# Optimization experiments

Measured on AMD Instinct MI355X. Metric: run time of the kernel, lower is better.

The kernel has to match this reference:

```python
import jax, jax.numpy as jnp
import numpy as np

EPS = 1e-5
NUM_HEADS = 8
KEY_DIM = 32
V_DIM = 128  # att_ratio * key_dim

def bn2d(x, g, b, m, v):
    # inference BatchNorm2d on NCHW
    s = g * jax.lax.rsqrt(v + EPS)
    return x * s[None, :, None, None] + (b - m * s)[None, :, None, None]

def conv1x1(x, w):
    # w: [out_c, in_c], x: [B,C,H,W]
    return jnp.einsum('oc,bchw->bohw', w, x)

def _bn_params(key, c):
    k1, k2, k3, k4 = jax.random.split(key, 4)
    g = jax.random.uniform(k1, (c,), jnp.float32, 0.5, 1.5)
    b = jax.random.normal(k2, (c,), jnp.float32) * 0.1
    m = jax.random.normal(k3, (c,), jnp.float32) * 0.1
    v = jax.random.uniform(k4, (c,), jnp.float32, 0.5, 1.5)
    return g, b, m, v

def setup_inputs() -> dict:
    key = jax.random.key(0)
    ks = jax.random.split(key, 12)
    inp_dim, out_dim = 256, 512
    kv_out = (KEY_DIM + V_DIM) * NUM_HEADS      # 1280
    q_out = KEY_DIM * NUM_HEADS                 # 256
    merge_dim = V_DIM * NUM_HEADS               # 1024
    hid = out_dim * 2                            # mlp_ratio=2 -> 1024
    d = {}
    d['x'] = jax.random.normal(ks[0], (32, inp_dim, 32, 32), jnp.float32)
    d['kv_w'] = jax.random.normal(ks[1], (kv_out, inp_dim), jnp.float32) * 0.02
    d['kv_g'], d['kv_b'], d['kv_m'], d['kv_v'] = _bn_params(ks[2], kv_out)
    d['q_w'] = jax.random.normal(ks[3], (q_out, inp_dim), jnp.float32) * 0.02
    d['q_g'], d['q_b'], d['q_m'], d['q_v'] = _bn_params(ks[4], q_out)
    d['mg_w'] = jax.random.normal(ks[5], (out_dim, merge_dim), jnp.float32) * 0.02
    d['mg_g'], d['mg_b'], d['mg_m'], d['mg_v'] = _bn_params(ks[6], out_dim)
    d['fc1_w'] = jax.random.normal(ks[7], (hid, out_dim), jnp.float32) * 0.02
    d['bn1_g'], d['bn1_b'], d['bn1_m'], d['bn1_v'] = _bn_params(ks[8], hid)
    d['fc2_w'] = jax.random.normal(ks[9], (out_dim, hid), jnp.float32) * 0.02
    d['bn2_g'], d['bn2_b'], d['bn2_m'], d['bn2_v'] = _bn_params(ks[10], out_dim)
    return d

def reference(x, kv_w, kv_g, kv_b, kv_m, kv_v, q_w, q_g, q_b, q_m, q_v,
              mg_w, mg_g, mg_b, mg_m, mg_v,
              fc1_w, bn1_g, bn1_b, bn1_m, bn1_v,
              fc2_w, bn2_g, bn2_b, bn2_m, bn2_v):
    B, C, H, W = x.shape
    scale = KEY_DIM ** (-0.5)
    # kv projection: conv1x1 + BN, then split per head into k, v
    kv = bn2d(conv1x1(x, kv_w), kv_g, kv_b, kv_m, kv_v)
    kv = kv.reshape(B, NUM_HEADS, KEY_DIM + V_DIM, H * W)
    k = kv[:, :, :KEY_DIM]   # [B,h,Dk,N]
    v = kv[:, :, KEY_DIM:]   # [B,h,Dv,N]
    # query subsampling: AvgPool2d(kernel=1, stride=2) == strided slice
    xq = x[:, :, ::2, ::2]
    q = bn2d(conv1x1(xq, q_w), q_g, q_b, q_m, q_v)
    q = q.reshape(B, NUM_HEADS, KEY_DIM, -1)  # [B,h,Dk,Nq]
    # att = q^T @ k * scale, softmax over keys
    att = jax.nn.softmax(jnp.einsum('bhdq,bhdn->bhqn', q, k) * scale, axis=-1)
    h2, w2 = (H + 1) // 2, (W + 1) // 2
    # out = v @ att^T, channel-first layout
    o = jnp.einsum('bhvn,bhqn->bhvq', v, att).reshape(B, NUM_HEADS * V_DIM, h2, w2)
    # merge: GELU -> conv1x1 -> BN
    o = bn2d(conv1x1(jax.nn.gelu(o, approximate=False), mg_w), mg_g, mg_b, mg_m, mg_v)
    # ConvMlp: conv1x1 -> BN -> GELU -> conv1x1 -> BN
    y = bn2d(conv1x1(o, fc1_w), bn1_g, bn1_b, bn1_m, bn1_v)
    y = jax.nn.gelu(y, approximate=False)
    y = bn2d(conv1x1(y, fc2_w), bn2_g, bn2_b, bn2_m, bn2_v)
    return y
```

## Files before the change

kernel.cpp:

```cpp
#include <hip/hip_runtime.h>
#include <hip/hip_bf16.h>

#define BN_EPS 1e-5f

typedef short s8v __attribute__((ext_vector_type(8)));
typedef float f4v __attribute__((ext_vector_type(4)));
typedef unsigned short u16x8 __attribute__((ext_vector_type(8)));

__device__ __forceinline__ float bu2f(unsigned short u) {
    union { unsigned int i; float f; } c; c.i = ((unsigned int)u) << 16; return c.f;
}
__device__ __forceinline__ unsigned short f2bu(float f) {
    union { float f; unsigned int i; } c; c.f = f;
    unsigned int i = c.i;
    i += 0x7FFFu + ((i >> 16) & 1u);
    return (unsigned short)(i >> 16);
}
__device__ __forceinline__ float gelu_exact(float x) {
    return 0.5f * x * (1.0f + erff(x * 0.70710678118654752f));
}
__device__ __forceinline__ float ldin(const void* p, long i, bool f32) {
    return f32 ? ((const float*)p)[i] : bu2f(((const unsigned short*)p)[i]);
}
__device__ __forceinline__ s8v ldfrag(const unsigned short* p) {
    return *reinterpret_cast<const s8v*>(p);
}
__device__ __forceinline__ void gld16(const void* g, void* l) {
    __builtin_amdgcn_global_load_lds(
        (const __attribute__((address_space(1))) unsigned int*)g,
        (__attribute__((address_space(3))) unsigned int*)l, 16, 0, 0);
}
__device__ __forceinline__ s8v ldsw32(const unsigned short* T, int row, int quad) {
    return *reinterpret_cast<const s8v*>(T + row * 32 + ((quad ^ ((row >> 1) & 3)) << 3));
}
__device__ __forceinline__ s8v ldsw64(const unsigned short* T, int row, int chunk) {
    return *reinterpret_cast<const s8v*>(T + row * 64 + ((chunk ^ (row & 7)) << 3));
}
__device__ __forceinline__ int detect_f32(const unsigned short* xu) {
    int insane = 0;
    for (int i = 0; i < 128; ++i) {
        unsigned int e = (xu[i] >> 7) & 0xFFu;
        if (e == 255u || (e != 0u && (e < 96u || e > 159u))) ++insane;
    }
    return (insane >= 16) ? 1 : 0;
}

__global__ __launch_bounds__(256)
void prep_kernel(const void* __restrict__ x,
                 const void* __restrict__ w0, const void* __restrict__ w1,
                 const void* __restrict__ w2, const void* __restrict__ w3,
                 const void* __restrict__ w4,
                 unsigned short* __restrict__ wdst,
                 unsigned short* __restrict__ xT,
                 unsigned short* __restrict__ xqT,
                 int* __restrict__ dtf)
{
    __shared__ int sflag;
    __shared__ unsigned short T[64][66];
    const int tid = threadIdx.x;
    const int bid = blockIdx.x;
    if (tid == 0) {
        int fl = detect_f32((const unsigned short*)x);
        sflag = fl;
        if (bid == 0) *dtf = fl;
    }
    __syncthreads();
    const bool f = (sflag != 0);

    if (bid < 960) {
        long idx = (long)bid * 2048 + tid * 8;
        const void* s; long off;
        if      (idx <  327680L) { s = w0; off = idx; }
        else if (idx <  393216L) { s = w1; off = idx - 327680L; }
        else if (idx <  917504L) { s = w2; off = idx - 393216L; }
        else if (idx < 1441792L) { s = w3; off = idx - 917504L; }
        else                     { s = w4; off = idx - 1441792L; }
        u16x8 pk;
        if (f) {
            float4 a = *((const float4*)((const float*)s + off));
            float4 b = *((const float4*)((const float*)s + off + 4));
            pk[0]=f2bu(a.x); pk[1]=f2bu(a.y); pk[2]=f2bu(a.z); pk[3]=f2bu(a.w);
            pk[4]=f2bu(b.x); pk[5]=f2bu(b.y); pk[6]=f2bu(b.z); pk[7]=f2bu(b.w);
        } else {
            pk = *((const u16x8*)((const unsigned short*)s + off));
        }
        *reinterpret_cast<u16x8*>(wdst + idx) = pk;
        return;
    }
    int b, c0, n0, ND; bool SUBS;
    if (bid < 3008) { int t = bid - 960;  b = t >> 6; int r = t & 63;
                      c0 = (r >> 4) * 64; n0 = (r & 15) * 64; ND = 1024; SUBS = false; }
    else            { int t = bid - 3008; b = t >> 4; int r = t & 15;
                      c0 = (r >> 2) * 64; n0 = (r & 3) * 64;  ND = 256;  SUBS = true; }
    unsigned short* dst = SUBS ? xqT : xT;
    {
        int nn = tid & 63, cq = tid >> 6;
        int n = n0 + nn;
        int sc = SUBS ? ((n >> 4) * 64 + (n & 15) * 2) : n;
        long base = ((long)b * 256 + c0 + cq * 16) * 1024 + sc;
        #pragma unroll
        for (int i = 0; i < 16; ++i)
            T[nn][cq * 16 + i] = f2bu(ldin(x, base + (long)i * 1024, f));
    }
    __syncthreads();
    {
        int cc = tid & 63, nq = tid >> 6;
        #pragma unroll
        for (int i = 0; i < 16; ++i) {
            int nn = nq * 16 + i;
            dst[((long)b * ND + n0 + nn) * 256 + c0 + cc] = T[nn][cc];
        }
    }
}

template<int OUT_MODE, bool DO_GELU, bool PRESCALE, int BM>
__global__ __launch_bounds__(256)
void mfma_gemm(const unsigned short* __restrict__ A,
               const unsigned short* __restrict__ B,
               const void* __restrict__ gg, const void* __restrict__ bb,
               const void* __restrict__ mmu, const void* __restrict__ vv,
               void* __restrict__ out0, unsigned short* __restrict__ out1,
               int M, int K, int N, const int* __restrict__ dtflag)
{
    constexpr int NF = (BM == 128) ? 4 : 2;
    constexpr int MP0 = 72;
    constexpr int MP1 = 136;
    constexpr int LOOPSH = BM * 64 + 128 * 64;
    constexpr int TILESH = (OUT_MODE == 1) ? 128 * MP1 : ((OUT_MODE == 0) ? 128 * MP0 : 0);
    constexpr int SMS = (LOOPSH > TILESH) ? LOOPSH : TILESH;
    __shared__ __align__(16) unsigned short smem[SMS];
    __shared__ float sS[BM], sO[BM];
    unsigned short* As = smem;
    unsigned short* Bs = smem + BM * 64;
    unsigned short* Tt = smem;

    const bool wf = (*dtflag != 0);
    const int tid = threadIdx.x;
    const int lane = tid & 63;
    const int wave = tid >> 6;
    const int quad = lane >> 4;
    const int l15  = lane & 15;
    const int wm2 = (BM == 128) ? (wave >> 1) * 64 : 0;
    const int wn2 = (BM == 128) ? (wave & 1) * 64 : wave * 32;
    const int b  = blockIdx.z;
    const int bm = blockIdx.y * BM;
    const int bn = blockIdx.x * 128;

    if (tid < BM) {
        int m = bm + tid;
        float g  = ldin(gg,  m, wf), be = ldin(bb,  m, wf);
        float mu = ldin(mmu, m, wf), va = ldin(vv,  m, wf);
        float s = g * rsqrtf(va + BN_EPS);
        float o = be - mu * s;
        if (PRESCALE) { s *= 0.17677669529663687f; o *= 0.17677669529663687f; }
        sS[tid] = s; sO[tid] = o;
    }

    const unsigned short* Bb = B + (long)b * N * K;

    f4v acc[4][NF];
    #pragma unroll
    for (int i = 0; i < 4; ++i)
        #pragma unroll
        for (int j = 0; j < NF; ++j) acc[i][j] = (f4v){0.f, 0.f, 0.f, 0.f};

    const int lr8 = lane >> 3;
    const int lc8 = lane & 7;

    for (int k0 = 0; k0 < K; k0 += 64) {
        #pragma unroll
        for (int j = 0; j < (BM == 128 ? 4 : 2); ++j) {
            int base = wave * (BM == 128 ? 32 : 16) + j * 8;
            int r = base + lr8;
            gld16(A + (long)(bm + r) * K + k0 + ((lc8 ^ (r & 7)) << 3),
                  As + base * 64);
        }
        #pragma unroll
        for (int j = 0; j < 4; ++j) {
            int base = wave * 32 + j * 8;
            int r = base + lr8;
            gld16(Bb + (long)(bn + r) * K + k0 + ((lc8 ^ (r & 7)) << 3),
                  Bs + base * 64);
        }
        __syncthreads();

        #pragma unroll
        for (int sk = 0; sk < 2; ++sk) {
            s8v af[4], bfr[NF];
            #pragma unroll
            for (int i = 0; i < 4; ++i)
                af[i]  = ldsw64(As, wm2 + i * 16 + l15, sk * 4 + quad);
            #pragma unroll
            for (int j = 0; j < NF; ++j)
                bfr[j] = ldsw64(Bs, wn2 + j * 16 + l15, sk * 4 + quad);
            #pragma unroll
            for (int i = 0; i < 4; ++i)
                #pragma unroll
                for (int j = 0; j < NF; ++j)
                    acc[i][j] = __builtin_amdgcn_mfma_f32_16x16x32_bf16(
                        af[i], bfr[j], acc[i][j], 0, 0, 0);
        }
        __syncthreads();
    }

    #pragma unroll
    for (int i = 0; i < 4; ++i) {
        int m0l = wm2 + i * 16 + quad * 4;
        int m0  = bm + m0l;
        float s0 = sS[m0l + 0], o0 = sO[m0l + 0];
        float s1 = sS[m0l + 1], o1 = sO[m0l + 1];
        float s2 = sS[m0l + 2], o2 = sO[m0l + 2];
        float s3 = sS[m0l + 3], o3 = sO[m0l + 3];
        #pragma unroll
        for (int j = 0; j < NF; ++j) {
            int nl = wn2 + j * 16 + l15;
            int n = bn + nl;
            float v0 = acc[i][j][0] * s0 + o0;
            float v1 = acc[i][j][1] * s1 + o1;
            float v2 = acc[i][j][2] * s2 + o2;
            float v3 = acc[i][j][3] * s3 + o3;
            if (DO_GELU) {
                v0 = gelu_exact(v0); v1 = gelu_exact(v1);
                v2 = gelu_exact(v2); v3 = gelu_exact(v3);
            }
            if (OUT_MODE == 0) {
                ushort4 pk; pk.x = f2bu(v0); pk.y = f2bu(v1);
                pk.z = f2bu(v2); pk.w = f2bu(v3);
                *reinterpret_cast<ushort4*>(&Tt[nl * MP0 + m0l]) = pk;
            } else if (OUT_MODE == 1) {
                int h = m0 / 160, seg = m0 - h * 160;
                if (seg < 32) {
                    ushort4 pk; pk.x = f2bu(v0); pk.y = f2bu(v1);
                    pk.z = f2bu(v2); pk.w = f2bu(v3);
                    *reinterpret_cast<ushort4*>(
                        (unsigned short*)out0 + ((long)(b * 8 + h) * 1024 + n) * 32 + seg) = pk;
                } else {
                    Tt[(m0l + 0) * MP1 + nl] = f2bu(v0);
                    Tt[(m0l + 1) * MP1 + nl] = f2bu(v1);
                    Tt[(m0l + 2) * MP1 + nl] = f2bu(v2);
                    Tt[(m0l + 3) * MP1 + nl] = f2bu(v3);
                }
            } else if (OUT_MODE == 2) {
                int b2 = n >> 8, nl2 = n & 255;
                long ob = ((long)b2 * M + m0) * 256 + nl2;
                if (wf) {
                    ((float*)out0)[ob + 0L * 256] = v0;
                    ((float*)out0)[ob + 1L * 256] = v1;
                    ((float*)out0)[ob + 2L * 256] = v2;
                    ((float*)out0)[ob + 3L * 256] = v3;
                } else {
                    ((unsigned short*)out0)[ob + 0L * 256] = f2bu(v0);
                    ((unsigned short*)out0)[ob + 1L * 256] = f2bu(v1);
                    ((unsigned short*)out0)[ob + 2L * 256] = f2bu(v2);
                    ((unsigned short*)out0)[ob + 3L * 256] = f2bu(v3);
                }
            } else {
                int h = m0 >> 5;
                ushort4 pk; pk.x = f2bu(v0); pk.y = f2bu(v1);
                pk.z = f2bu(v2); pk.w = f2bu(v3);
                *reinterpret_cast<ushort4*>(
                    (unsigned short*)out0 + ((long)(b * 8 + h) * 256 + n) * 32 + (m0 & 31)) = pk;
            }
        }
    }

    if (OUT_MODE == 0) {
        __syncthreads();
        long ob = ((long)b * N + bn) * M + bm;
        #pragma unroll
        for (int c = 0; c < BM / 16; ++c) {
            int cc = c * 256 + tid;
            int n = cc >> 3, mc = (cc & 7) << 3;
            *reinterpret_cast<u16x8*>((unsigned short*)out0 + ob + (long)n * M + mc) =
                *reinterpret_cast<const u16x8*>(&Tt[n * MP0 + mc]);
        }
    } else if (OUT_MODE == 1) {
        __syncthreads();
        int h0 = (bm + 159) / 160;
        int ks = h0 * 160;
        bool hasK = (ks < bm + 128);
        int kl = hasK ? (ks - bm) : 128;
        int nrows = hasK ? 96 : 128;
        for (int c = tid; c < nrows * 16; c += 256) {
            int row = c >> 4, ch = (c & 15) << 3;
            int ml = (row < kl) ? row : (row + 32);
            int m = bm + ml;
            int hh = m / 160, seg = m - hh * 160;
            *reinterpret_cast<u16x8*>(out1 +
                (((long)(b * 8 + hh) * 128) + (seg - 32)) * (long)N + bn + ch) =
                *reinterpret_cast<const u16x8*>(&Tt[ml * MP1 + ch]);
        }
    }
}

__global__ __launch_bounds__(512, 4)
void attn_mfma(const unsigned short* __restrict__ kvK,
               const unsigned short* __restrict__ kvV,
               const unsigned short* __restrict__ qh,
               unsigned short* __restrict__ goT)
{
    __shared__ unsigned short Ks[64 * 32];
    __shared__ unsigned short Vs[128 * 64];
    __shared__ unsigned short Ps[128][72];
    __shared__ float redS[128];

    const int tid = threadIdx.x;
    const int lane = tid & 63;
    const int wave = tid >> 6;
    const int quad = lane >> 4;
    const int l15  = lane & 15;
    const int h    = blockIdx.x;
    const int b    = blockIdx.y;
    const int q0   = blockIdx.z * 128;
    const int wq   = wave * 16;

    const unsigned short* Qb = qh  + (long)(b * 8 + h) * 256 * 32;
    const unsigned short* Kb = kvK + (long)(b * 8 + h) * 1024 * 32;
    const unsigned short* Vb = kvV + (long)(b * 8 + h) * 128 * 1024;

    s8v qf = ldfrag(Qb + (long)(q0 + wq + l15) * 32 + quad * 8);

    f4v o[8];
    #pragma unroll
    for (int i = 0; i < 8; ++i) o[i] = (f4v){0.f, 0.f, 0.f, 0.f};
    float rs[4] = {0.f, 0.f, 0.f, 0.f};

    for (int n0 = 0; n0 < 1024; n0 += 64) {
        if (wave < 4) {
            int r = wave * 16 + (lane >> 2);
            int c = (lane & 3) ^ ((r >> 1) & 3);
            gld16(Kb + (long)(n0 + r) * 32 + (c << 3), Ks + wave * 16 * 32);
        }
        {
            int rb = wave * 16;
            int r0 = rb + (lane >> 3), r1 = r0 + 8;
            int s  = lane & 7;
            gld16(Vb + (long)r0 * 1024 + n0 + ((s ^ (r0 & 7)) << 3), Vs + rb * 64);
            gld16(Vb + (long)r1 * 1024 + n0 + ((s ^ (r1 & 7)) << 3), Vs + (rb + 8) * 64);
        }
        __syncthreads();

        #pragma unroll
        for (int j = 0; j < 4; ++j) {
            s8v kf = ldsw32(Ks, j * 16 + l15, quad);
            f4v z = (f4v){0.f, 0.f, 0.f, 0.f};
            f4v sa = __builtin_amdgcn_mfma_f32_16x16x32_bf16(qf, kf, z, 0, 0, 0);
            #pragma unroll
            for (int r = 0; r < 4; ++r) {
                float p = __expf(fminf(sa[r], 30.f));
                rs[r] += p;
                Ps[wq + quad * 4 + r][j * 16 + l15] = f2bu(p);
            }
        }
        #pragma unroll
        for (int ks = 0; ks < 2; ++ks) {
            s8v pf = ldfrag(&Ps[wq + l15][ks * 32 + quad * 8]);
            #pragma unroll
            for (int i = 0; i < 8; ++i) {
                s8v vf = ldsw64(Vs, i * 16 + l15, ks * 4 + quad);
                o[i] = __builtin_amdgcn_mfma_f32_16x16x32_bf16(vf, pf, o[i], 0, 0, 0);
            }
        }
        __syncthreads();
    }

    #pragma unroll
    for (int r = 0; r < 4; ++r) {
        float s = rs[r];
        s += __shfl_xor(s, 1);
        s += __shfl_xor(s, 2);
        s += __shfl_xor(s, 4);
        s += __shfl_xor(s, 8);
        if (l15 == 0) redS[wq + quad * 4 + r] = s;
    }
    float linv = 1.0f / redS[wq + l15];
    int q = q0 + wq + l15;
    #pragma unroll
    for (int i = 0; i < 8; ++i) {
        ushort4 pk;
        pk.x = f2bu(gelu_exact(o[i][0] * linv));
        pk.y = f2bu(gelu_exact(o[i][1] * linv));
        pk.z = f2bu(gelu_exact(o[i][2] * linv));
        pk.w = f2bu(gelu_exact(o[i][3] * linv));
        *reinterpret_cast<ushort4*>(
            goT + ((long)b * 256 + q) * 1024 + h * 128 + i * 16 + quad * 4) = pk;
    }
}

extern "C" void kernel_launch(void* const* d_in, const int* in_sizes, int n_in,
                              void* d_out, int out_size, void* d_ws, size_t ws_size,
                              hipStream_t stream)
{
    const void* x     = d_in[0];
    const void* kv_w  = d_in[1];
    const void* kv_g  = d_in[2];  const void* kv_b  = d_in[3];
    const void* kv_m  = d_in[4];  const void* kv_v  = d_in[5];
    const void* q_w   = d_in[6];
    const void* q_g   = d_in[7];  const void* q_b   = d_in[8];
    const void* q_m   = d_in[9];  const void* q_v   = d_in[10];
    const void* mg_w  = d_in[11];
    const void* mg_g  = d_in[12]; const void* mg_b  = d_in[13];
    const void* mg_m  = d_in[14]; const void* mg_v  = d_in[15];
    const void* fc1_w = d_in[16];
    const void* bn1_g = d_in[17]; const void* bn1_b = d_in[18];
    const void* bn1_m = d_in[19]; const void* bn1_v = d_in[20];
    const void* fc2_w = d_in[21];
    const void* bn2_g = d_in[22]; const void* bn2_b = d_in[23];
    const void* bn2_m = d_in[24]; const void* bn2_v = d_in[25];

    unsigned short* ws  = (unsigned short*)d_ws;
    int*            dtf = (int*)d_ws;
    unsigned short* wsW  = ws + 8;
    unsigned short* wKV  = wsW;
    unsigned short* wQ   = wsW + 327680L;
    unsigned short* wMG  = wsW + 393216L;
    unsigned short* wFC1 = wsW + 917504L;
    unsigned short* wFC2 = wsW + 1441792L;
    unsigned short* xT   = ws + 1966088L;
    unsigned short* goT  = xT;
    unsigned short* xqT  = ws + 10354696L;
    unsigned short* qhb  = ws + 12451848L;
    unsigned short* kvK  = ws + 14549000L;
    unsigned short* kvV  = ws + 22937608L;
    unsigned short* y1T  = kvV;
    unsigned short* y2T  = kvV + 4194304L;

    dim3 blk(256, 1, 1);

    prep_kernel<<<3520, blk, 0, stream>>>(
        x, kv_w, q_w, mg_w, fc1_w, fc2_w, wsW, xT, xqT, dtf);

    mfma_gemm<3, false, true, 64><<<dim3(2, 4, 32), blk, 0, stream>>>(
        wQ, xqT, q_g, q_b, q_m, q_v, qhb, nullptr, 256, 256, 256, dtf);

    mfma_gemm<1, false, false, 128><<<dim3(8, 10, 32), blk, 0, stream>>>(
        wKV, xT, kv_g, kv_b, kv_m, kv_v, kvK, kvV, 1280, 256, 1024, dtf);

    attn_mfma<<<dim3(8, 32, 2), dim3(512, 1, 1), 0, stream>>>(kvK, kvV, qhb, goT);

    mfma_gemm<0, false, false, 64><<<dim3(64, 8, 1), blk, 0, stream>>>(
        wMG, goT, mg_g, mg_b, mg_m, mg_v, y1T, nullptr, 512, 1024, 8192, dtf);

    mfma_gemm<0, true, false, 64><<<dim3(64, 16, 1), blk, 0, stream>>>(
        wFC1, y1T, bn1_g, bn1_b, bn1_m, bn1_v, y2T, nullptr, 1024, 512, 8192, dtf);

    mfma_gemm<2, false, false, 64><<<dim3(64, 8, 1), blk, 0, stream>>>(
        wFC2, y2T, bn2_g, bn2_b, bn2_m, bn2_v, d_out, nullptr, 512, 1024, 8192, dtf);
}
```

Before: 308.0 us.

## Double-buffer K/V tiles in attention kernel to overlap loads with MFMA

Splits the K and V shared-memory tiles into two buffers and issues the global-to-LDS loads for the next key block before computing on the current one. The aim is to hide global memory latency behind the QK and PV MFMA work. Loop-invariant address arithmetic is also hoisted out of the loop. In exchange, LDS use rises by about 20KB per block, which may lower occupancy at 4 blocks per CU. Correctness depends on the existing end-of-loop barrier ordering the buffer reuse.

```diff
diff --git a/kernel.cpp b/kernel.cpp
--- a/kernel.cpp
+++ b/kernel.cpp
@@ -299,8 +299,8 @@
                const unsigned short* __restrict__ qh,
                unsigned short* __restrict__ goT)
 {
-    __shared__ unsigned short Ks[64 * 32];
-    __shared__ unsigned short Vs[128 * 64];
+    __shared__ unsigned short Ks[2][64 * 32];
+    __shared__ unsigned short Vs[2][128 * 64];
     __shared__ unsigned short Ps[128][72];
     __shared__ float redS[128];
 
@@ -320,29 +320,41 @@
 
     s8v qf = ldfrag(Qb + (long)(q0 + wq + l15) * 32 + quad * 8);
 
+    const unsigned short* pK = Kb;
+    if (wave < 4) {
+        int r = wave * 16 + (lane >> 2);
+        int c = (lane & 3) ^ ((r >> 1) & 3);
+        pK = Kb + (long)r * 32 + (c << 3);
+    }
+    const int rb = wave * 16;
+    const int r0 = rb + (lane >> 3), r1 = r0 + 8;
+    const int sl = lane & 7;
+    const unsigned short* pV0 = Vb + (long)r0 * 1024 + ((sl ^ (r0 & 7)) << 3);
+    const unsigned short* pV1 = Vb + (long)r1 * 1024 + ((sl ^ (r1 & 7)) << 3);
+
     f4v o[8];
     #pragma unroll
     for (int i = 0; i < 8; ++i) o[i] = (f4v){0.f, 0.f, 0.f, 0.f};
     float rs[4] = {0.f, 0.f, 0.f, 0.f};
 
-    for (int n0 = 0; n0 < 1024; n0 += 64) {
-        if (wave < 4) {
-            int r = wave * 16 + (lane >> 2);
-            int c = (lane & 3) ^ ((r >> 1) & 3);
-            gld16(Kb + (long)(n0 + r) * 32 + (c << 3), Ks + wave * 16 * 32);
-        }
-        {
-            int rb = wave * 16;
-            int r0 = rb + (lane >> 3), r1 = r0 + 8;
-            int s  = lane & 7;
-            gld16(Vb + (long)r0 * 1024 + n0 + ((s ^ (r0 & 7)) << 3), Vs + rb * 64);
-            gld16(Vb + (long)r1 * 1024 + n0 + ((s ^ (r1 & 7)) << 3), Vs + (rb + 8) * 64);
-        }
-        __syncthreads();
+    if (wave < 4) gld16(pK, &Ks[0][wave * 16 * 32]);
+    gld16(pV0, &Vs[0][rb * 64]);
+    gld16(pV1, &Vs[0][(rb + 8) * 64]);
+    __syncthreads();
+
+    for (int t = 0; t < 16; ++t) {
+        const int cur = t & 1;
+        if (t < 15) {
+            const int nxt = cur ^ 1;
+            const long adv = (long)(t + 1) * 64;
+            if (wave < 4) gld16(pK + adv * 32, &Ks[nxt][wave * 16 * 32]);
+            gld16(pV0 + adv, &Vs[nxt][rb * 64]);
+            gld16(pV1 + adv, &Vs[nxt][(rb + 8) * 64]);
+        }
 
         #pragma unroll
         for (int j = 0; j < 4; ++j) {
-            s8v kf = ldsw32(Ks, j * 16 + l15, quad);
+            s8v kf = ldsw32(&Ks[cur][0], j * 16 + l15, quad);
             f4v z = (f4v){0.f, 0.f, 0.f, 0.f};
             f4v sa = __builtin_amdgcn_mfma_f32_16x16x32_bf16(qf, kf, z, 0, 0, 0);
             #pragma unroll
@@ -357,7 +369,7 @@
             s8v pf = ldfrag(&Ps[wq + l15][ks * 32 + quad * 8]);
             #pragma unroll
             for (int i = 0; i < 8; ++i) {
-                s8v vf = ldsw64(Vs, i * 16 + l15, ks * 4 + quad);
+                s8v vf = ldsw64(&Vs[cur][0], i * 16 + l15, ks * 4 + quad);
                 o[i] = __builtin_amdgcn_mfma_f32_16x16x32_bf16(vf, pf, o[i], 0, 0, 0);
             }
         }
```

Result: no change. 304.4 us (-1.2%).
